# Kernel optimization log

Hardware: AMD Instinct MI355X
Metric: run time of the kernel (lower is better)

The kernel has to match this reference:

```python
import jax, jax.numpy as jnp
import numpy as np

B, N, K_NN, H, IN_DIM, OUT_DIM = 32, 1024, 16, 64, 4, 2
START = 2 * H   # EdgeConv MLP input width (cat[x_i, x_j - x_i])
MID = 3 * H // 2


def _elu(x):
    return jax.nn.elu(x)


def _lin_init(key, fan_in, fan_out):
    k1, k2 = jax.random.split(key)
    lim = 1.0 / np.sqrt(fan_in)
    W = jax.random.uniform(k1, (fan_in, fan_out), minval=-lim, maxval=lim, dtype=jnp.float32)
    b = jax.random.uniform(k2, (fan_out,), minval=-lim, maxval=lim, dtype=jnp.float32)
    return W, b


def setup_inputs():
    key = jax.random.key(0)
    ks = jax.random.split(key, 11)
    inp = {
        "x": jax.random.normal(ks[0], (B, N, IN_DIM), dtype=jnp.float32),
        "norm": jnp.array([1e-3, 1e-1, 1.0 / 3.15, 1.0 / 3000.0], dtype=jnp.float32),
    }
    dims = [("in1", IN_DIM, H // 2), ("in2", H // 2, H), ("in3", H, H),
            ("c1a", START, MID), ("c1b", MID, H),
            ("c2a", START, MID), ("c2b", MID, H),
            ("o1", H, H), ("o2", H, H // 2), ("o3", H // 2, OUT_DIM)]
    for i, (nm, fi, fo) in enumerate(dims):
        W, b = _lin_init(ks[i + 1], fi, fo)
        inp[nm + "_W"] = W
        inp[nm + "_b"] = b
    return inp


def _pdist2(x):
    # squared pairwise distances per graph: [B,n,n]
    x2 = jnp.sum(x * x, -1)
    d2 = x2[:, :, None] + x2[:, None, :] - 2.0 * jnp.einsum('bnh,bmh->bnm', x, x)
    return jnp.maximum(d2, 0.0)


def _knn(x, valid, k):
    # knn_graph(loop=False) restricted to valid (non-padded) target columns
    b, n, _ = x.shape
    d2 = _pdist2(jax.lax.stop_gradient(x))
    bad = jnp.eye(n, dtype=bool)[None] | (~valid)[:, None, :]
    d2 = jnp.where(bad, jnp.inf, d2)
    _, idx = jax.lax.top_k(-d2, k)                      # [B,n,k] neighbor ids
    bi = jnp.arange(b)[:, None, None]
    ni = jnp.arange(n)[None, :, None]
    Kd = jnp.zeros((b, n, n), bool).at[bi, ni, idx].set(True)   # dense kNN adjacency
    return idx, Kd


def _edge_mlp(e, W1, b1, W2, b2):
    return _elu(_elu(e @ W1 + b1) @ W2 + b2)


def _edgeconv(x, valid, idx, Kd, W1, b1, W2, b2):
    # EdgeConv(aggr='add') over to_undirected(knn_graph): message nn([x_i, x_j - x_i])
    b, n, h = x.shape
    xj = jax.vmap(lambda xg, ig: xg[ig])(x, idx)        # [B,n,k,h] gathered neighbors
    xi = jnp.broadcast_to(x[:, :, None, :], xj.shape)
    agg = _edge_mlp(jnp.concatenate([xi, xj - xi], -1), W1, b1, W2, b2).sum(2)
    # reverse edges added by to_undirected; coalesce drops duplicates of mutual kNN pairs
    mutual = jnp.take_along_axis(jnp.swapaxes(Kd, 1, 2), idx, axis=2)  # [B,n,k]
    w_rev = ((~mutual) & valid[:, :, None]).astype(x.dtype)
    msg_rev = _edge_mlp(jnp.concatenate([xj, xi - xj], -1), W1, b1, W2, b2) * w_rev[..., None]
    seg = (jnp.arange(b)[:, None, None] * n + idx).reshape(-1)
    agg_rev = jax.ops.segment_sum(msg_rev.reshape(-1, h), seg, num_segments=b * n).reshape(b, n, h)
    return agg + agg_rev


def _norm_cut_w(x, A):
    # normalized_cut_2d: ||x_i - x_j|| * (1/deg_i + 1/deg_j) on edges, -inf elsewhere
    dist = jnp.sqrt(_pdist2(x))
    invdeg = 1.0 / A.sum(-1).astype(x.dtype)
    cut = dist * (invdeg[:, :, None] + invdeg[:, None, :])
    return jnp.where(A, cut, -jnp.inf)


def _graclus(Wm):
    # greedy heavy-edge matching (deterministic node order), like graclus
    n = Wm.shape[-1]

    def match_one(Wg):
        def body(i, st):
            unmatched, cluster = st
            wi = jnp.where(unmatched, Wg[i], -jnp.inf)
            j = jnp.argmax(wi)
            ok = unmatched[i] & jnp.isfinite(wi[j])
            r = jnp.minimum(i, j)
            cluster = jnp.where(ok, cluster.at[i].set(r).at[j].set(r), cluster)
            unmatched = unmatched.at[i].set(False)
            unmatched = jnp.where(ok, unmatched.at[j].set(False), unmatched)
            return unmatched, cluster

        return jax.lax.fori_loop(0, n, body, (jnp.ones(n, bool), jnp.arange(n)))[1]

    return jax.vmap(match_one)(jax.lax.stop_gradient(Wm))


def _max_pool(x, cluster):
    # max over each cluster; representative = min node index; padded slots masked
    b, n, h = x.shape
    pooled = jax.vmap(lambda xg, cg: jax.ops.segment_max(xg, cg, num_segments=n))(x, cluster)
    counts = jax.vmap(lambda cg: jnp.zeros(n, jnp.int32).at[cg].add(1))(cluster)
    valid = counts > 0
    return jnp.where(valid[..., None], pooled, 0.0), valid


def _forward(x, norm, in1_W, in1_b, in2_W, in2_b, in3_W, in3_b,
             c1a_W, c1a_b, c1b_W, c1b_b, c2a_W, c2a_b, c2b_W, c2b_b,
             o1_W, o1_b, o2_W, o2_b, o3_W, o3_b):
    h0 = x * norm
    h0 = _elu(_elu(_elu(h0 @ in1_W + in1_b) @ in2_W + in2_b) @ in3_W + in3_b)
    valid0 = jnp.ones(h0.shape[:2], bool)
    idx1, K1 = _knn(h0, valid0, K_NN)
    h1 = _edgeconv(h0, valid0, idx1, K1, c1a_W, c1a_b, c1b_W, c1b_b)
    A1 = K1 | jnp.swapaxes(K1, 1, 2)
    cl = _graclus(_norm_cut_w(jax.lax.stop_gradient(h1), A1))
    h1p, valid1 = _max_pool(h1, cl)
    idx2, K2 = _knn(h1p, valid1, K_NN)
    h2 = _edgeconv(h1p, valid1, idx2, K2, c2a_W, c2a_b, c2b_W, c2b_b)
    # 2nd graclus max_pool_x followed by global_max_pool == global max over valid nodes
    g = jnp.max(jnp.where(valid1[..., None], h2, -jnp.inf), axis=1)   # [B,H]
    return _elu(_elu(g @ o1_W + o1_b) @ o2_W + o2_b) @ o3_W + o3_b


def reference(x, norm, in1_W, in1_b, in2_W, in2_b, in3_W, in3_b,
              c1a_W, c1a_b, c1b_W, c1b_b, c2a_W, c2a_b, c2b_W, c2b_b,
              o1_W, o1_b, o2_W, o2_b, o3_W, o3_b):
    return _forward(x, norm, in1_W, in1_b, in2_W, in2_b, in3_W, in3_b,
                    c1a_W, c1a_b, c1b_W, c1b_b, c2a_W, c2a_b, c2b_W, c2b_b,
                    o1_W, o1_b, o2_W, o2_b, o3_W, o3_b)
```

## Files before the change

kernel.cpp:

```cpp
#include <hip/hip_runtime.h>
#include <cmath>


#define DEVI __device__ __forceinline__
constexpr int B_   = 32;
constexpr int N_   = 1024;
constexpr int NN   = B_ * N_;
constexpr int NCH  = 8;
constexpr int CHW  = 128;
constexpr int ECAP = 128;

#define INFF (__builtin_huge_valf())

DEVI float elu_(float x)  { return x > 0.f ? x : expm1f(x); }
DEVI float eluf(float x)  { return x > 0.f ? x : __expf(x) - 1.f; }

__global__ __launch_bounds__(256) void k_input(
    const float* __restrict__ x, const float* __restrict__ nrm,
    const float* __restrict__ w1, const float* __restrict__ b1,
    const float* __restrict__ w2, const float* __restrict__ b2,
    const float* __restrict__ w3, const float* __restrict__ b3,
    float* __restrict__ h0, float* __restrict__ x2a)
{
  __shared__ float s1[128], sb1[32], s2[2048], sb2[64], s3[4096], sb3[64];
  int tid = threadIdx.x;
  for (int t = tid; t < 128; t += 256) s1[t] = w1[t];
  if (tid < 32) sb1[tid] = b1[tid];
  for (int t = tid; t < 2048; t += 256) s2[t] = w2[t];
  if (tid < 64) sb2[tid] = b2[tid];
  for (int t = tid; t < 4096; t += 256) s3[t] = w3[t];
  if (tid < 64) sb3[tid] = b3[tid];
  __syncthreads();
  int n = blockIdx.x * 256 + tid;
  float xi[4];
#pragma unroll
  for (int d = 0; d < 4; d++) xi[d] = x[n * 4 + d] * nrm[d];
  float a1[32];
#pragma unroll
  for (int c = 0; c < 32; c++) {
    float a = sb1[c];
#pragma unroll
    for (int d = 0; d < 4; d++) a += xi[d] * s1[d * 32 + c];
    a1[c] = elu_(a);
  }
  float a2[64];
#pragma unroll
  for (int c = 0; c < 64; c++) {
    float a = sb2[c];
#pragma unroll
    for (int d = 0; d < 32; d++) a += a1[d] * s2[d * 64 + c];
    a2[c] = elu_(a);
  }
  float ss = 0.f;
#pragma unroll
  for (int c = 0; c < 64; c++) {
    float a = sb3[c];
#pragma unroll
    for (int d = 0; d < 64; d++) a += a2[d] * s3[d * 64 + c];
    a = elu_(a);
    h0[n * 64 + c] = a;
    ss += a * a;
  }
  x2a[n] = ss;
}

__global__ __launch_bounds__(256) void k_knn(
    const float4* __restrict__ X4, const float* __restrict__ X2,
    const unsigned* __restrict__ vbits, const int* __restrict__ vrows,
    float* __restrict__ pd, unsigned short* __restrict__ pix)
{
  __shared__ float xs[CHW * 64];
  __shared__ float xs2[CHW];
  __shared__ unsigned vm[32];
  int bid = blockIdx.x;
  int swz = (bid & 7) * 128 + (bid >> 3);
  int b  = swz >> 5;
  int rt = (swz >> 3) & 3;
  int ch = swz & 7;
  int tid = threadIdx.x;
  int j0 = ch * CHW;
  for (int t = tid; t < CHW * 16; t += 256) {
    int r = t >> 4, q = t & 15;
    float4 v = X4[(b * N_ + j0 + r) * 16 + q];
    *reinterpret_cast<float4*>(&xs[r * 64 + q * 4]) = v;
  }
  for (int t = tid; t < CHW; t += 256) xs2[t] = X2[b * N_ + j0 + t];
  for (int t = tid; t < 32; t += 256) vm[t] = vbits ? vbits[b * 32 + t] : 0xFFFFFFFFu;
  __syncthreads();
  int i = rt * 256 + tid;
  int gi = b * N_ + i;
  if (vrows && !vrows[gi]) return;
  float4 xi4[16];
#pragma unroll
  for (int q = 0; q < 16; q++) xi4[q] = X4[gi * 16 + q];
  float x2i = X2[gi];
  float topd[16]; int topi[16];
#pragma unroll
  for (int q = 0; q < 16; q++) { topd[q] = INFF; topi[q] = 0xFFFF; }
  for (int jj = 0; jj < CHW; ++jj) {
    int j = j0 + jj;
    if (j == i) continue;
    if (!((vm[j >> 5] >> (j & 31)) & 1u)) continue;
    const float4* xr = reinterpret_cast<const float4*>(&xs[jj * 64]);
    float dot = 0.f;
#pragma unroll
    for (int q = 0; q < 16; q++) {
      float4 v = xr[q];
      dot += xi4[q].x * v.x + xi4[q].y * v.y + xi4[q].z * v.z + xi4[q].w * v.w;
    }
    float d2 = fmaxf(x2i + xs2[jj] - 2.f * dot, 0.f);
    if (d2 < topd[15]) {
      topd[15] = d2; topi[15] = j;
#pragma unroll
      for (int p = 15; p > 0; --p) {
        if (topd[p] < topd[p - 1]) {
          float td = topd[p]; topd[p] = topd[p - 1]; topd[p - 1] = td;
          int   ti = topi[p]; topi[p] = topi[p - 1]; topi[p - 1] = ti;
        }
      }
    }
  }
  size_t base = ((size_t)gi * NCH + ch) * 16;
#pragma unroll
  for (int q = 0; q < 16; q++) { pd[base + q] = topd[q]; pix[base + q] = (unsigned short)topi[q]; }
}

__global__ __launch_bounds__(64) void k_merge(
    const float* __restrict__ pd, const unsigned short* __restrict__ pix,
    const int* __restrict__ vrows,
    unsigned* __restrict__ Kb, unsigned* __restrict__ KTb)
{
  __shared__ unsigned lbm[64][33];
  int tid = threadIdx.x;
  int gi = blockIdx.x * 64 + tid;
  int b = gi >> 10, i = gi & 1023;
  if (vrows && !vrows[gi]) return;
#pragma unroll
  for (int w = 0; w < 32; w++) lbm[tid][w] = 0u;
  float topd[16]; int topi[16];
#pragma unroll
  for (int q = 0; q < 16; q++) { topd[q] = INFF; topi[q] = 0; }
  for (int s = 0; s < NCH; ++s) {
    size_t base = ((size_t)gi * NCH + s) * 16;
#pragma unroll 1
    for (int q = 0; q < 16; q++) {
      float d = pd[base + q];
      if (!(d < topd[15])) break;
      topd[15] = d; topi[15] = pix[base + q];
#pragma unroll
      for (int p = 15; p > 0; --p) {
        if (topd[p] < topd[p - 1]) {
          float td = topd[p]; topd[p] = topd[p - 1]; topd[p - 1] = td;
          int   ti = topi[p]; topi[p] = topi[p - 1]; topi[p - 1] = ti;
        }
      }
    }
  }
#pragma unroll
  for (int q = 0; q < 16; q++) {
    int j = topi[q];
    lbm[tid][j >> 5] |= (1u << (j & 31));
    atomicOr(&KTb[((size_t)b * N_ + j) * 32 + (i >> 5)], 1u << (i & 31));
  }
#pragma unroll
  for (int w = 0; w < 32; w++) Kb[(size_t)gi * 32 + w] = lbm[tid][w];
}

__global__ __launch_bounds__(256) void k_elist(
    const unsigned* __restrict__ Kb, const unsigned* __restrict__ KTb,
    unsigned short* __restrict__ E, int* __restrict__ ecnt, float* __restrict__ invdeg)
{
  int gi = blockIdx.x * 256 + threadIdx.x;
  unsigned short* e = E + (size_t)gi * ECAP;
  int n = 0;
  for (int w = 0; w < 32; w++) {
    unsigned m = Kb[(size_t)gi * 32 + w] | KTb[(size_t)gi * 32 + w];
    while (m) {
      int bit = __ffs(m) - 1; m &= m - 1;
      if (n < ECAP) e[n] = (unsigned short)(w * 32 + bit);
      n++;
    }
  }
  ecnt[gi] = n < ECAP ? n : ECAP;
  if (invdeg) invdeg[gi] = 1.f / (float)n;
}

__global__ __launch_bounds__(256) void k_uv(
    const float* __restrict__ X, const float* __restrict__ W1, const float* __restrict__ b1,
    float* __restrict__ wb, float* __restrict__ vb)
{
  __shared__ float wc[64 * 96], wv[64 * 96];
  int tid = threadIdx.x;
  for (int t = tid; t < 64 * 96; t += 256) {
    int d = t / 96, c = t - d * 96;
    float hv = W1[(d + 64) * 96 + c];
    wv[t] = hv;
    wc[t] = W1[d * 96 + c] - hv;
  }
  __syncthreads();
  int n = blockIdx.x * 256 + tid;
  float xi[64];
#pragma unroll
  for (int q = 0; q < 16; q++) {
    float4 v = reinterpret_cast<const float4*>(X)[n * 16 + q];
    xi[q * 4] = v.x; xi[q * 4 + 1] = v.y; xi[q * 4 + 2] = v.z; xi[q * 4 + 3] = v.w;
  }
#pragma unroll 1
  for (int c4 = 0; c4 < 24; c4++) {
    float aw0 = b1[c4 * 4 + 0], aw1 = b1[c4 * 4 + 1], aw2 = b1[c4 * 4 + 2], aw3 = b1[c4 * 4 + 3];
    float av0 = 0.f, av1 = 0.f, av2 = 0.f, av3 = 0.f;
#pragma unroll
    for (int d = 0; d < 64; d++) {
      float4 c = *reinterpret_cast<const float4*>(&wc[d * 96 + c4 * 4]);
      float4 v = *reinterpret_cast<const float4*>(&wv[d * 96 + c4 * 4]);
      float xd = xi[d];
      aw0 += xd * c.x; aw1 += xd * c.y; aw2 += xd * c.z; aw3 += xd * c.w;
      av0 += xd * v.x; av1 += xd * v.y; av2 += xd * v.z; av3 += xd * v.w;
    }
    wb[(size_t)n * 96 + c4 * 4 + 0] = aw0; wb[(size_t)n * 96 + c4 * 4 + 1] = aw1;
    wb[(size_t)n * 96 + c4 * 4 + 2] = aw2; wb[(size_t)n * 96 + c4 * 4 + 3] = aw3;
    vb[(size_t)n * 96 + c4 * 4 + 0] = av0; vb[(size_t)n * 96 + c4 * 4 + 1] = av1;
    vb[(size_t)n * 96 + c4 * 4 + 2] = av2; vb[(size_t)n * 96 + c4 * 4 + 3] = av3;
  }
}

__global__ __launch_bounds__(256) void k_conv(
    const float* __restrict__ wbuf, const float* __restrict__ vbuf,
    const unsigned short* __restrict__ E, const int* __restrict__ ecnt,
    const int* __restrict__ vrows,
    const float* __restrict__ W2, const float* __restrict__ b2,
    float* __restrict__ out, float* __restrict__ x2out)
{
  __shared__ float w2s[96 * 64];
  __shared__ float b2s[64];
  __shared__ float wds[64 * 100];
  int tid = threadIdx.x;
  int bid = blockIdx.x;
  int swz = (bid & 7) * 64 + (bid >> 3);
  int dst0 = swz * 64;
  for (int t = tid; t < 96 * 64; t += 256) w2s[t] = W2[t];
  if (tid < 64) b2s[tid] = b2[tid];
  for (int t = tid; t < 64 * 96; t += 256) {
    int l = t / 96, c = t - l * 96;
    wds[l * 100 + c] = wbuf[(size_t)(dst0 + l) * 96 + c];
  }
  __syncthreads();
  int dl = tid >> 2, p = tid & 3;
  int dst = dst0 + dl;
  if (vrows && !vrows[dst]) return;
  int cnt = ecnt[dst];
  const unsigned short* e = E + (size_t)dst * ECAP;
  int gb = dst & ~(N_ - 1);
  float agg[16];
#pragma unroll
  for (int o = 0; o < 16; o++) agg[o] = 0.f;

#pragma unroll 1
  for (int k = 0; k < cnt; k += 2) {
    bool hasB = (k + 1 < cnt);
    int sA = gb + e[k];
    int sB = hasB ? gb + e[k + 1] : sA;
    const float4* vA = reinterpret_cast<const float4*>(vbuf + (size_t)sA * 96);
    const float4* vB = reinterpret_cast<const float4*>(vbuf + (size_t)sB * 96);
    float sa[16], sb_[16];
#pragma unroll
    for (int o = 0; o < 16; o++) { sa[o] = b2s[p * 16 + o]; sb_[o] = sa[o]; }
#pragma unroll 1
    for (int c4 = 0; c4 < 24; c4++) {
      float4 wv = *reinterpret_cast<const float4*>(&wds[dl * 100 + c4 * 4]);
      float4 a4 = vA[c4];
      float4 b4 = vB[c4];
      float tA0 = eluf(wv.x + a4.x), tA1 = eluf(wv.y + a4.y),
            tA2 = eluf(wv.z + a4.z), tA3 = eluf(wv.w + a4.w);
      float tB0 = eluf(wv.x + b4.x), tB1 = eluf(wv.y + b4.y),
            tB2 = eluf(wv.z + b4.z), tB3 = eluf(wv.w + b4.w);
      const float* wr = &w2s[(c4 * 4) * 64 + p * 16];
#pragma unroll
      for (int o4 = 0; o4 < 4; o4++) {
        float4 w0 = *reinterpret_cast<const float4*>(wr + 0 * 64 + o4 * 4);
        float4 w1 = *reinterpret_cast<const float4*>(wr + 1 * 64 + o4 * 4);
        float4 w2 = *reinterpret_cast<const float4*>(wr + 2 * 64 + o4 * 4);
        float4 w3 = *reinterpret_cast<const float4*>(wr + 3 * 64 + o4 * 4);
        sa [o4*4+0] += tA0*w0.x + tA1*w1.x + tA2*w2.x + tA3*w3.x;
        sa [o4*4+1] += tA0*w0.y + tA1*w1.y + tA2*w2.y + tA3*w3.y;
        sa [o4*4+2] += tA0*w0.z + tA1*w1.z + tA2*w2.z + tA3*w3.z;
        sa [o4*4+3] += tA0*w0.w + tA1*w1.w + tA2*w2.w + tA3*w3.w;
        sb_[o4*4+0] += tB0*w0.x + tB1*w1.x + tB2*w2.x + tB3*w3.x;
        sb_[o4*4+1] += tB0*w0.y + tB1*w1.y + tB2*w2.y + tB3*w3.y;
        sb_[o4*4+2] += tB0*w0.z + tB1*w1.z + tB2*w2.z + tB3*w3.z;
        sb_[o4*4+3] += tB0*w0.w + tB1*w1.w + tB2*w2.w + tB3*w3.w;
      }
    }
#pragma unroll
    for (int o = 0; o < 16; o++) agg[o] += eluf(sa[o]);
    if (hasB) {
#pragma unroll
      for (int o = 0; o < 16; o++) agg[o] += eluf(sb_[o]);
    }
  }
  float4* o4p = reinterpret_cast<float4*>(out + (size_t)dst * 64 + p * 16);
#pragma unroll
  for (int q = 0; q < 4; q++)
    o4p[q] = make_float4(agg[q*4], agg[q*4+1], agg[q*4+2], agg[q*4+3]);
  if (x2out) {
    float s = 0.f;
#pragma unroll
    for (int o = 0; o < 16; o++) s += agg[o] * agg[o];
    s += __shfl_xor(s, 1, 64);
    s += __shfl_xor(s, 2, 64);
    if (p == 0) x2out[dst] = s;
  }
}

__global__ __launch_bounds__(256) void k_wgt(
    const float* __restrict__ h1, const float* __restrict__ x2h,
    const float* __restrict__ invdeg, const unsigned short* __restrict__ E,
    const int* __restrict__ ecnt, unsigned* __restrict__ cw)
{
  int bid = blockIdx.x;
  int swz = (bid & 7) * 16 + (bid >> 3);
  int gi = swz * 256 + threadIdx.x;
  int base = gi & ~(N_ - 1);
  float xi[64];
#pragma unroll
  for (int q = 0; q < 16; q++) {
    float4 v = reinterpret_cast<const float4*>(h1)[gi * 16 + q];
    xi[q * 4] = v.x; xi[q * 4 + 1] = v.y; xi[q * 4 + 2] = v.z; xi[q * 4 + 3] = v.w;
  }
  float x2i = x2h[gi];
  float idi = invdeg[gi];
  int cnt = ecnt[gi];
  const unsigned short* e = E + (size_t)gi * ECAP;
  unsigned* crow = cw + (size_t)gi * ECAP;
#pragma unroll 1
  for (int n = 0; n < cnt; n++) {
    int j = base + e[n];
    const float4* r = reinterpret_cast<const float4*>(h1 + (size_t)j * 64);
    float dot = 0.f;
#pragma unroll
    for (int q = 0; q < 16; q++) {
      float4 v = r[q];
      dot += xi[q * 4] * v.x + xi[q * 4 + 1] * v.y + xi[q * 4 + 2] * v.z + xi[q * 4 + 3] * v.w;
    }
    float d2 = fmaxf(x2i + x2h[j] - 2.f * dot, 0.f);
    float wgt = sqrtf(d2) * (idi + invdeg[j]);
    crow[n] = __float_as_uint(wgt);
  }
}

__global__ __launch_bounds__(64) void k_graclus(
    const unsigned* __restrict__ cw, const unsigned short* __restrict__ E,
    const int* __restrict__ ecnt, int* __restrict__ cluster, int* __restrict__ partner)
{
  __shared__ unsigned char um[N_];
  int b = blockIdx.x, lane = threadIdx.x;
  int g0 = b * N_;
  size_t r0 = (size_t)g0 * ECAP;
  for (int t = lane; t < N_; t += 64) { um[t] = 1; cluster[g0 + t] = t; partner[g0 + t] = -1; }
  __syncthreads();
  unsigned wA0 = cw[r0 + lane], wA1 = cw[r0 + 64 + lane];
  unsigned jA0 = E[r0 + lane],  jA1 = E[r0 + 64 + lane];
  int cA = ecnt[g0];
  unsigned wB0 = cw[r0 + ECAP + lane], wB1 = cw[r0 + ECAP + 64 + lane];
  unsigned jB0 = E[r0 + ECAP + lane],  jB1 = E[r0 + ECAP + 64 + lane];
  int cB = ecnt[g0 + 1];

  auto step = [&](int i, unsigned w0, unsigned w1, unsigned j0, unsigned j1, int cc) {
    if (!um[i]) return;
    unsigned long long k0 = 0ull, k1 = 0ull;
    if (lane < cc      && um[j0 & (N_ - 1)]) k0 = ((unsigned long long)w0 << 32) | (unsigned)~j0;
    if (lane + 64 < cc && um[j1 & (N_ - 1)]) k1 = ((unsigned long long)w1 << 32) | (unsigned)~j1;
    unsigned long long kk = k0 > k1 ? k0 : k1;
#pragma unroll
    for (int off = 32; off; off >>= 1) {
      unsigned long long o = __shfl_xor(kk, off, 64);
      if (o > kk) kk = o;
    }
    if (lane == 0) {
      um[i] = 0;
      if (kk) {
        int j = (int)(~(unsigned)(kk & 0xFFFFFFFFull));
        um[j] = 0;
        int r = i < j ? i : j;
        int o = i ^ j ^ r;
        cluster[g0 + o] = r;
        partner[g0 + r] = o;
      }
    }
    asm volatile("s_waitcnt lgkmcnt(0)" ::: "memory");
  };

  for (int i = 0; i < N_; i += 2) {
    step(i, wA0, wA1, jA0, jA1, cA);
    if (i + 2 < N_) {
      size_t rr = r0 + (size_t)(i + 2) * ECAP;
      wA0 = cw[rr + lane]; wA1 = cw[rr + 64 + lane];
      jA0 = E[rr + lane];  jA1 = E[rr + 64 + lane];
      cA = ecnt[g0 + i + 2];
    }
    step(i + 1, wB0, wB1, jB0, jB1, cB);
    if (i + 3 < N_) {
      size_t rr = r0 + (size_t)(i + 3) * ECAP;
      wB0 = cw[rr + lane]; wB1 = cw[rr + 64 + lane];
      jB0 = E[rr + lane];  jB1 = E[rr + 64 + lane];
      cB = ecnt[g0 + i + 3];
    }
  }
}

__global__ __launch_bounds__(256) void k_maxpool(
    const float* __restrict__ h1, const int* __restrict__ cluster, const int* __restrict__ partner,
    float* __restrict__ h1p, float* __restrict__ x2p, int* __restrict__ valid1,
    unsigned* __restrict__ vbits)
{
  int gi = blockIdx.x * 256 + threadIdx.x;
  int b = gi >> 10, i = gi & 1023;
  if (cluster[gi] == i) {
    int p = partner[gi];
    float s = 0.f;
#pragma unroll
    for (int q = 0; q < 16; q++) {
      float4 a = reinterpret_cast<const float4*>(h1)[gi * 16 + q];
      if (p >= 0) {
        float4 c = reinterpret_cast<const float4*>(h1)[(b * N_ + p) * 16 + q];
        a.x = fmaxf(a.x, c.x); a.y = fmaxf(a.y, c.y); a.z = fmaxf(a.z, c.z); a.w = fmaxf(a.w, c.w);
      }
      reinterpret_cast<float4*>(h1p)[gi * 16 + q] = a;
      s += a.x * a.x + a.y * a.y + a.z * a.z + a.w * a.w;
    }
    x2p[gi] = s; valid1[gi] = 1;
    atomicOr(&vbits[b * 32 + (i >> 5)], 1u << (i & 31));
  } else {
    float4 z = make_float4(0.f, 0.f, 0.f, 0.f);
#pragma unroll
    for (int q = 0; q < 16; q++) reinterpret_cast<float4*>(h1p)[gi * 16 + q] = z;
    x2p[gi] = 0.f; valid1[gi] = 0;
  }
}

__global__ __launch_bounds__(256) void k_final(
    const float* __restrict__ h2, const int* __restrict__ valid1,
    const float* __restrict__ o1W, const float* __restrict__ o1b,
    const float* __restrict__ o2W, const float* __restrict__ o2b,
    const float* __restrict__ o3W, const float* __restrict__ o3b,
    float* __restrict__ out)
{
  __shared__ float gm[4][64], g[64], l1[64], l2[32];
  int b = blockIdx.x, tid = threadIdx.x;
  int d = tid & 63, r = tid >> 6;
  float m = -INFF;
  for (int i = r; i < N_; i += 4) {
    if (valid1[b * N_ + i]) m = fmaxf(m, h2[(size_t)(b * N_ + i) * 64 + d]);
  }
  gm[r][d] = m;
  __syncthreads();
  if (tid < 64) g[d] = fmaxf(fmaxf(gm[0][d], gm[1][d]), fmaxf(gm[2][d], gm[3][d]));
  __syncthreads();
  if (tid < 64) {
    float a = o1b[tid];
    for (int c = 0; c < 64; c++) a += g[c] * o1W[c * 64 + tid];
    l1[tid] = elu_(a);
  }
  __syncthreads();
  if (tid < 32) {
    float a2 = o2b[tid];
    for (int c = 0; c < 64; c++) a2 += l1[c] * o2W[c * 32 + tid];
    l2[tid] = elu_(a2);
  }
  __syncthreads();
  if (tid < 2) {
    float a3 = o3b[tid];
    for (int c = 0; c < 32; c++) a3 += l2[c] * o3W[c * 2 + tid];
    out[b * 2 + tid] = a3;
  }
}

extern "C" void kernel_launch(void* const* d_in, const int* in_sizes, int n_in,
                              void* d_out, int out_size, void* d_ws, size_t ws_size,
                              hipStream_t stream)
{
  const float* x    = (const float*)d_in[0];
  const float* nrm  = (const float*)d_in[1];
  const float* in1W = (const float*)d_in[2];  const float* in1b = (const float*)d_in[3];
  const float* in2W = (const float*)d_in[4];  const float* in2b = (const float*)d_in[5];
  const float* in3W = (const float*)d_in[6];  const float* in3b = (const float*)d_in[7];
  const float* c1aW = (const float*)d_in[8];  const float* c1ab = (const float*)d_in[9];
  const float* c1bW = (const float*)d_in[10]; const float* c1bb = (const float*)d_in[11];
  const float* c2aW = (const float*)d_in[12]; const float* c2ab = (const float*)d_in[13];
  const float* c2bW = (const float*)d_in[14]; const float* c2bb = (const float*)d_in[15];
  const float* o1W  = (const float*)d_in[16]; const float* o1b  = (const float*)d_in[17];
  const float* o2W  = (const float*)d_in[18]; const float* o2b  = (const float*)d_in[19];
  const float* o3W  = (const float*)d_in[20]; const float* o3b  = (const float*)d_in[21];

  constexpr size_t O_H0    = 0;
  constexpr size_t O_X2A   = O_H0    + (size_t)NN * 64 * 4;
  constexpr size_t O_U     = O_X2A   + (size_t)NN * 4;
  constexpr size_t O_K     = O_U     + (size_t)NN * NCH * 16 * 6;
  constexpr size_t O_KT    = O_K     + (size_t)NN * 32 * 4;
  constexpr size_t O_H1    = O_KT    + (size_t)NN * 32 * 4;
  constexpr size_t O_X2H   = O_H1    + (size_t)NN * 64 * 4;
  constexpr size_t O_IDG   = O_X2H   + (size_t)NN * 4;
  constexpr size_t O_ECNT  = O_IDG   + (size_t)NN * 4;
  constexpr size_t O_CLU   = O_ECNT  + (size_t)NN * 4;
  constexpr size_t O_PAR   = O_CLU   + (size_t)NN * 4;
  constexpr size_t O_VAL   = O_PAR   + (size_t)NN * 4;
  constexpr size_t O_VBITS = O_VAL   + (size_t)NN * 4;
  constexpr size_t O_E     = O_VBITS + (size_t)B_ * 32 * 4;
  constexpr size_t TOTAL   = O_E     + (size_t)NN * ECAP * 2;
  if (ws_size < TOTAL) return;

  char* w = (char*)d_ws;
  float*          h0   = (float*)(w + O_H0);
  float*          x2a  = (float*)(w + O_X2A);
  float*          pdp  = (float*)(w + O_U);
  unsigned short* pip  = (unsigned short*)(w + O_U + (size_t)NN * NCH * 16 * 4);
  float*          wb   = (float*)(w + O_U);
  float*          vb   = (float*)(w + O_U + (size_t)NN * 96 * 4);
  unsigned*       cwt  = (unsigned*)(w + O_U);
  unsigned*       Kb   = (unsigned*)(w + O_K);
  unsigned*       KTb  = (unsigned*)(w + O_KT);
  float*          h1   = (float*)(w + O_H1);
  float*          x2h  = (float*)(w + O_X2H);
  float*          idg  = (float*)(w + O_IDG);
  int*            ecnt = (int*)(w + O_ECNT);
  int*            clu  = (int*)(w + O_CLU);
  int*            par  = (int*)(w + O_PAR);
  int*            val  = (int*)(w + O_VAL);
  unsigned*       vbits= (unsigned*)(w + O_VBITS);
  unsigned short* E    = (unsigned short*)(w + O_E);
  float* h1p = h0;
  float* x2p = x2a;
  float* h2  = h1;

  k_input<<<NN / 256, 256, 0, stream>>>(x, nrm, in1W, in1b, in2W, in2b, in3W, in3b, h0, x2a);
  k_knn<<<B_ * 32, 256, 0, stream>>>((const float4*)h0, x2a, nullptr, nullptr, pdp, pip);
  hipMemsetAsync(KTb, 0, (size_t)NN * 32 * 4, stream);
  k_merge<<<NN / 64, 64, 0, stream>>>(pdp, pip, nullptr, Kb, KTb);
  k_elist<<<NN / 256, 256, 0, stream>>>(Kb, KTb, E, ecnt, idg);
  k_uv<<<NN / 256, 256, 0, stream>>>(h0, c1aW, c1ab, wb, vb);
  k_conv<<<NN / 64, 256, 0, stream>>>(wb, vb, E, ecnt, nullptr, c1bW, c1bb, h1, x2h);
  k_wgt<<<NN / 256, 256, 0, stream>>>(h1, x2h, idg, E, ecnt, cwt);
  k_graclus<<<B_, 64, 0, stream>>>(cwt, E, ecnt, clu, par);
  hipMemsetAsync(vbits, 0, (size_t)B_ * 32 * 4, stream);
  k_maxpool<<<NN / 256, 256, 0, stream>>>(h1, clu, par, h1p, x2p, val, vbits);
  k_knn<<<B_ * 32, 256, 0, stream>>>((const float4*)h1p, x2p, vbits, val, pdp, pip);
  hipMemsetAsync(Kb, 0, (size_t)NN * 32 * 4 * 2, stream);
  k_merge<<<NN / 64, 64, 0, stream>>>(pdp, pip, val, Kb, KTb);
  k_elist<<<NN / 256, 256, 0, stream>>>(Kb, KTb, E, ecnt, nullptr);
  k_uv<<<NN / 256, 256, 0, stream>>>(h1p, c2aW, c2ab, wb, vb);
  k_conv<<<NN / 64, 256, 0, stream>>>(wb, vb, E, ecnt, val, c2bW, c2bb, h2, nullptr);
  k_final<<<B_, 256, 0, stream>>>(h2, val, o1W, o1b, o2W, o2b, o3W, o3b, (float*)d_out);
}
```

Before: 1.851 ms.

## Presort edge rows by weight so graclus picks partner via ballot

Adds a parallel bitonic sort kernel that orders each node's edge list by descending cut weight, with ties broken by index. The sequential graclus loop then takes the first still-unmatched neighbour using a ballot and lowest-lane test, instead of running a 64-bit shuffle max reduction per node. It also stops loading weights in the serial loop and prefetches four rows ahead instead of two. The cost is an extra kernel launch plus the sort work, and the sort writes E in place even though E is read later by the second edgeconv stage.

New measurement: 1.957 ms. +5.7%, slower.

```diff
diff --git a/kernel.cpp b/kernel.cpp
--- a/kernel.cpp
+++ b/kernel.cpp
@@ -348,64 +348,97 @@
   }
 }
 
+__global__ __launch_bounds__(256) void k_sort(
+    const unsigned* __restrict__ cw, const unsigned short* __restrict__ E0,
+    const int* __restrict__ ecnt, unsigned short* __restrict__ E)
+{
+  int node = (blockIdx.x * 256 + threadIdx.x) >> 6;
+  int lane = threadIdx.x & 63;
+  int cnt = ecnt[node];
+  size_t rb = (size_t)node * ECAP;
+  unsigned long long a = 0ull, b = 0ull;
+  if (lane < cnt)
+    a = ((unsigned long long)cw[rb + lane] << 32) | (unsigned)(~(unsigned)E0[rb + lane]);
+  if (lane + 64 < cnt)
+    b = ((unsigned long long)cw[rb + 64 + lane] << 32) | (unsigned)(~(unsigned)E0[rb + 64 + lane]);
+#pragma unroll
+  for (int k = 2; k <= 128; k <<= 1) {
+#pragma unroll
+    for (int jj = k >> 1; jj > 0; jj >>= 1) {
+      if (jj == 64) {
+        unsigned long long mx = a > b ? a : b;
+        b = a > b ? b : a;
+        a = mx;
+      } else {
+        unsigned long long oa = __shfl_xor(a, jj, 64);
+        bool low   = (lane & jj) == 0;
+        bool descA = (lane & k) == 0;
+        a = ((low == descA) == (a > oa)) ? a : oa;
+        unsigned long long ob = __shfl_xor(b, jj, 64);
+        bool descB = (((lane + 64) & k) == 0);
+        b = ((low == descB) == (b > ob)) ? b : ob;
+      }
+    }
+  }
+  E[rb + lane]      = (unsigned short)(~(unsigned)a);
+  E[rb + 64 + lane] = (unsigned short)(~(unsigned)b);
+}
+
 __global__ __launch_bounds__(64) void k_graclus(
-    const unsigned* __restrict__ cw, const unsigned short* __restrict__ E,
-    const int* __restrict__ ecnt, int* __restrict__ cluster, int* __restrict__ partner)
+    const unsigned short* __restrict__ E, const int* __restrict__ ecnt,
+    int* __restrict__ cluster, int* __restrict__ partner)
 {
   __shared__ unsigned char um[N_];
   int b = blockIdx.x, lane = threadIdx.x;
   int g0 = b * N_;
-  size_t r0 = (size_t)g0 * ECAP;
+  const unsigned short* Eg = E + (size_t)g0 * ECAP;
   for (int t = lane; t < N_; t += 64) { um[t] = 1; cluster[g0 + t] = t; partner[g0 + t] = -1; }
   __syncthreads();
-  unsigned wA0 = cw[r0 + lane], wA1 = cw[r0 + 64 + lane];
-  unsigned jA0 = E[r0 + lane],  jA1 = E[r0 + 64 + lane];
-  int cA = ecnt[g0];
-  unsigned wB0 = cw[r0 + ECAP + lane], wB1 = cw[r0 + ECAP + 64 + lane];
-  unsigned jB0 = E[r0 + ECAP + lane],  jB1 = E[r0 + ECAP + 64 + lane];
-  int cB = ecnt[g0 + 1];
-
-  auto step = [&](int i, unsigned w0, unsigned w1, unsigned j0, unsigned j1, int cc) {
-    if (!um[i]) return;
-    unsigned long long k0 = 0ull, k1 = 0ull;
-    if (lane < cc      && um[j0 & (N_ - 1)]) k0 = ((unsigned long long)w0 << 32) | (unsigned)~j0;
-    if (lane + 64 < cc && um[j1 & (N_ - 1)]) k1 = ((unsigned long long)w1 << 32) | (unsigned)~j1;
-    unsigned long long kk = k0 > k1 ? k0 : k1;
-#pragma unroll
-    for (int off = 32; off; off >>= 1) {
-      unsigned long long o = __shfl_xor(kk, off, 64);
-      if (o > kk) kk = o;
-    }
-    if (lane == 0) {
-      um[i] = 0;
-      if (kk) {
-        int j = (int)(~(unsigned)(kk & 0xFFFFFFFFull));
-        um[j] = 0;
-        int r = i < j ? i : j;
-        int o = i ^ j ^ r;
-        cluster[g0 + o] = r;
-        partner[g0 + r] = o;
-      }
-    }
+
+  int jA0, jA1, cA, jB0, jB1, cB, jC0, jC1, cC, jD0, jD1, cD;
+#define LOADROW(J0, J1, CN, row)                                                \
+  { size_t rb_ = (size_t)(row) * ECAP;                                          \
+    J0 = Eg[rb_ + lane] & (N_ - 1);                                             \
+    J1 = Eg[rb_ + 64 + lane] & (N_ - 1);                                        \
+    CN = ecnt[g0 + (row)]; }
+  LOADROW(jA0, jA1, cA, 0)
+  LOADROW(jB0, jB1, cB, 1)
+  LOADROW(jC0, jC1, cC, 2)
+  LOADROW(jD0, jD1, cD, 3)
+
+  unsigned long long below = (1ull << lane) - 1ull;
+
+  auto step = [&](int i, int j0, int j1, int cc) {
+    bool ui = um[i] != 0;
+    bool p0 = (lane < cc)      && ui && (um[j0] != 0);
+    bool p1 = (lane + 64 < cc) && ui && (um[j1] != 0);
+    unsigned long long m0 = __ballot(p0);
+    unsigned long long m1 = __ballot(p1);
+    bool w0 = p0 && !(m0 & below);
+    bool w1 = (m0 == 0ull) && p1 && !(m1 & below);
+    if (w0 | w1) {
+      int jw = w0 ? j0 : j1;
+      um[jw] = 0;
+      int r = i < jw ? i : jw;
+      int o = i ^ jw ^ r;
+      cluster[g0 + o] = r;
+      partner[g0 + r] = o;
+    }
+    if (lane == 0) um[i] = 0;
     asm volatile("s_waitcnt lgkmcnt(0)" ::: "memory");
   };
 
-  for (int i = 0; i < N_; i += 2) {
-    step(i, wA0, wA1, jA0, jA1, cA);
-    if (i + 2 < N_) {
-      size_t rr = r0 + (size_t)(i + 2) * ECAP;
-      wA0 = cw[rr + lane]; wA1 = cw[rr + 64 + lane];
-      jA0 = E[rr + lane];  jA1 = E[rr + 64 + lane];
-      cA = ecnt[g0 + i + 2];
-    }
-    step(i + 1, wB0, wB1, jB0, jB1, cB);
-    if (i + 3 < N_) {
-      size_t rr = r0 + (size_t)(i + 3) * ECAP;
-      wB0 = cw[rr + lane]; wB1 = cw[rr + 64 + lane];
-      jB0 = E[rr + lane];  jB1 = E[rr + 64 + lane];
-      cB = ecnt[g0 + i + 3];
-    }
-  }
+  for (int i = 0; i < N_; i += 4) {
+    step(i, jA0, jA1, cA);
+    if (i + 4 < N_) LOADROW(jA0, jA1, cA, i + 4)
+    step(i + 1, jB0, jB1, cB);
+    if (i + 5 < N_) LOADROW(jB0, jB1, cB, i + 5)
+    step(i + 2, jC0, jC1, cC);
+    if (i + 6 < N_) LOADROW(jC0, jC1, cC, i + 6)
+    step(i + 3, jD0, jD1, cD);
+    if (i + 7 < N_) LOADROW(jD0, jD1, cD, i + 7)
+  }
+#undef LOADROW
 }
 
 __global__ __launch_bounds__(256) void k_maxpool(
@@ -540,7 +573,8 @@
   k_uv<<<NN / 256, 256, 0, stream>>>(h0, c1aW, c1ab, wb, vb);
   k_conv<<<NN / 64, 256, 0, stream>>>(wb, vb, E, ecnt, nullptr, c1bW, c1bb, h1, x2h);
   k_wgt<<<NN / 256, 256, 0, stream>>>(h1, x2h, idg, E, ecnt, cwt);
-  k_graclus<<<B_, 64, 0, stream>>>(cwt, E, ecnt, clu, par);
+  k_sort<<<NN / 4, 256, 0, stream>>>(cwt, E, ecnt, E);
+  k_graclus<<<B_, 64, 0, stream>>>(E, ecnt, clu, par);
   hipMemsetAsync(vbits, 0, (size_t)B_ * 32 * 4, stream);
   k_maxpool<<<NN / 256, 256, 0, stream>>>(h1, clu, par, h1p, x2p, val, vbits);
   k_knn<<<B_ * 32, 256, 0, stream>>>((const float4*)h1p, x2p, vbits, val, pdp, pip);
```
